# Performance work log

Hardware: AMD Instinct MI355X
Metric: run time of the kernel (lower is better)

## Reference

```python
import jax, jax.numpy as jnp
import numpy as np

D_MODEL, D_STATE, EXPAND = 1024, 256, 2
BATCH, SEQ = 8, 2048


def setup_inputs() -> dict:
    key = jax.random.key(0)
    ks = jax.random.split(key, 7)
    s = 0.02
    return {
        "x": jax.random.normal(ks[0], (BATCH, SEQ, D_MODEL), jnp.float32),
        "W_in": jax.random.normal(ks[1], (D_MODEL, D_MODEL * EXPAND), jnp.float32) * s,
        "b_in": jax.random.normal(ks[2], (D_MODEL * EXPAND,), jnp.float32) * s,
        "W_state": jax.random.normal(ks[3], (D_MODEL * EXPAND, D_STATE), jnp.float32) * s,
        "b_state": jax.random.normal(ks[4], (D_STATE,), jnp.float32) * s,
        "W_out": jax.random.normal(ks[5], (D_STATE, D_MODEL), jnp.float32) * s,
        "b_out": jax.random.normal(ks[6], (D_MODEL,), jnp.float32) * s,
        "init_state": jnp.zeros((1, D_STATE), jnp.float32),
    }


def reference(x, W_in, b_in, W_state, b_state, W_out, b_out, init_state):
    # x: [B, T, D]
    x_proj = jax.nn.silu(jnp.einsum("btd,de->bte", x, W_in) + b_in)  # [B,T,2D]
    # state_proj depends only on x_proj, so batch the GEMM over all timesteps
    updates = jnp.einsum("bte,es->bts", x_proj, W_state) + b_state    # [B,T,S]
    updates_t = jnp.swapaxes(updates, 0, 1)                            # [T,B,S]
    state0 = jnp.broadcast_to(init_state, (x.shape[0], init_state.shape[1]))

    def step(state, u):
        new = jax.nn.silu(state + u)
        return new, new

    _, states = jax.lax.scan(step, state0, updates_t)  # [T,B,S]
    out = jnp.einsum("tbs,sd->tbd", states, W_out) + b_out  # [T,B,D]
    return jnp.swapaxes(out, 0, 1)  # [B,T,D]
```

## Files before the change

### kernel.cpp

```cpp
#include <hip/hip_runtime.h>
#include <cstdint>
#include <cstddef>

#define BATCH 8
#define SEQ   2048
#define DM    1024
#define DE    2048
#define DSZ   256
#define MROWS (BATCH*SEQ)
#define MCHUNK 8192

typedef _Float16 f16;
typedef _Float16 f16x4 __attribute__((ext_vector_type(4)));
typedef _Float16 f16x8 __attribute__((ext_vector_type(8)));
typedef float  f32x4  __attribute__((ext_vector_type(4)));

__device__ __forceinline__ void glds16(const void* gp, void* lp) {
  __builtin_amdgcn_global_load_lds(
      (const __attribute__((address_space(1))) void*)gp,
      (__attribute__((address_space(3))) void*)lp, 16, 0, 0);
}

__device__ __forceinline__ float silu_f(float x) {
  return x * __builtin_amdgcn_rcpf(1.0f + __expf(-x));
}

__device__ __forceinline__ int swz(int k8, int r) { return k8 ^ ((r >> 1) & 3); }

__global__ void split_x_k(const float* __restrict__ in, f16* __restrict__ oh,
                          f16* __restrict__ ol, int n) {
  int i = (blockIdx.x * blockDim.x + threadIdx.x) * 4;
  const int stride = gridDim.x * blockDim.x * 4;
  for (; i < n; i += stride) {
    float4 v = *(const float4*)(in + i);
    f16x4 h, l;
    h[0] = (f16)v.x; l[0] = (f16)(v.x - (float)h[0]);
    h[1] = (f16)v.y; l[1] = (f16)(v.y - (float)h[1]);
    h[2] = (f16)v.z; l[2] = (f16)(v.z - (float)h[2]);
    h[3] = (f16)v.w; l[3] = (f16)(v.w - (float)h[3]);
    *(f16x4*)(oh + i) = h;
    *(f16x4*)(ol + i) = l;
  }
}

__global__ void transpose_split_k(const float* __restrict__ in, f16* __restrict__ oh,
                                  f16* __restrict__ ol, int R, int C) {
  __shared__ float tile[32][33];
  const int c0 = blockIdx.x * 32, r0 = blockIdx.y * 32;
  const int tx = threadIdx.x, ty = threadIdx.y;
  #pragma unroll
  for (int i = 0; i < 4; ++i)
    tile[ty + i*8][tx] = in[(size_t)(r0 + ty + i*8) * C + c0 + tx];
  __syncthreads();
  #pragma unroll
  for (int i = 0; i < 4; ++i) {
    float v = tile[tx][ty + i*8];
    f16 h = (f16)v;
    size_t idx = (size_t)(c0 + ty + i*8) * R + r0 + tx;
    oh[idx] = h;
    ol[idx] = (f16)(v - (float)h);
  }
}

__global__ void transpose_cast_f16_k(const float* __restrict__ in, f16* __restrict__ out, int R, int C) {
  __shared__ float tile[32][33];
  const int c0 = blockIdx.x * 32, r0 = blockIdx.y * 32;
  const int tx = threadIdx.x, ty = threadIdx.y;
  #pragma unroll
  for (int i = 0; i < 4; ++i)
    tile[ty + i*8][tx] = in[(size_t)(r0 + ty + i*8) * C + c0 + tx];
  __syncthreads();
  #pragma unroll
  for (int i = 0; i < 4; ++i)
    out[(size_t)(c0 + ty + i*8) * R + r0 + tx] = (f16)tile[tx][ty + i*8];
}

__global__ __launch_bounds__(512) void gemm1_k(const f16* __restrict__ Ah, const f16* __restrict__ Al,
                                               const f16* __restrict__ Bh, const f16* __restrict__ Bl,
                                               const float* __restrict__ bias,
                                               f16* __restrict__ Ch, f16* __restrict__ Cl) {
  const int K = 1024, N = 2048;
  __shared__ f16 sAh[2][4096], sAl[2][4096], sBh[2][4096], sBl[2][4096];

  const int tid = threadIdx.x;
  const int w = tid >> 6, l = tid & 63;
  const int bid = blockIdx.x;
  const int xcd = bid & 7, loc = bid >> 3;
  const int mt = xcd * 8 + (loc & 7);
  const int nt = loc >> 3;
  const int bm = mt * 128, bn = nt * 128;
  const int wm = (w >> 2) * 64, wn = (w & 3) * 32;
  const int lr = l & 15, lq = l >> 4;

  const int r = tid >> 2, k8 = swz(tid & 3, r);
  const f16* pAh = Ah + (size_t)(bm + r) * K + k8 * 8;
  const f16* pAl = Al + (size_t)(bm + r) * K + k8 * 8;
  const f16* pBh = Bh + (size_t)(bn + r) * K + k8 * 8;
  const f16* pBl = Bl + (size_t)(bn + r) * K + k8 * 8;
  const int dst = tid * 8;

  int offA[4], offB[2];
  #pragma unroll
  for (int i = 0; i < 4; ++i) {
    const int row = wm + i*16 + lr;
    offA[i] = row * 32 + swz(lq, row) * 8;
  }
  #pragma unroll
  for (int j = 0; j < 2; ++j) {
    const int row = wn + j*16 + lr;
    offB[j] = row * 32 + swz(lq, row) * 8;
  }

  f32x4 acc[4][2] = {};

  glds16(pAh, &sAh[0][dst]); glds16(pAl, &sAl[0][dst]);
  glds16(pBh, &sBh[0][dst]); glds16(pBl, &sBl[0][dst]);
  pAh += 32; pAl += 32; pBh += 32; pBl += 32;
  __syncthreads();

  for (int kt = 0; kt < 32; ++kt) {
    const int cur = kt & 1;
    if (kt < 31) {
      const int nxt = cur ^ 1;
      glds16(pAh, &sAh[nxt][dst]); glds16(pAl, &sAl[nxt][dst]);
      glds16(pBh, &sBh[nxt][dst]); glds16(pBl, &sBl[nxt][dst]);
      pAh += 32; pAl += 32; pBh += 32; pBl += 32;
    }
    f16x8 ah[4], al[4], bh[2], bl[2];
    #pragma unroll
    for (int i = 0; i < 4; ++i) {
      ah[i] = *(const f16x8*)(&sAh[cur][0] + offA[i]);
      al[i] = *(const f16x8*)(&sAl[cur][0] + offA[i]);
    }
    #pragma unroll
    for (int j = 0; j < 2; ++j) {
      bh[j] = *(const f16x8*)(&sBh[cur][0] + offB[j]);
      bl[j] = *(const f16x8*)(&sBl[cur][0] + offB[j]);
    }
    __builtin_amdgcn_s_setprio(1);
    #pragma unroll
    for (int i = 0; i < 4; ++i)
      #pragma unroll
      for (int j = 0; j < 2; ++j) {
        acc[i][j] = __builtin_amdgcn_mfma_f32_16x16x32_f16(ah[i], bh[j], acc[i][j], 0, 0, 0);
        acc[i][j] = __builtin_amdgcn_mfma_f32_16x16x32_f16(ah[i], bl[j], acc[i][j], 0, 0, 0);
        acc[i][j] = __builtin_amdgcn_mfma_f32_16x16x32_f16(al[i], bh[j], acc[i][j], 0, 0, 0);
      }
    __builtin_amdgcn_s_setprio(0);
    __syncthreads();
  }

  #pragma unroll
  for (int j = 0; j < 2; ++j) {
    const int col = bn + wn + j*16 + lr;
    const float bv = bias[col];
    #pragma unroll
    for (int i = 0; i < 4; ++i)
      #pragma unroll
      for (int r4 = 0; r4 < 4; ++r4) {
        const int row = bm + wm + i*16 + lq*4 + r4;
        const float s = silu_f(acc[i][j][r4] + bv);
        const f16 h = (f16)s;
        const size_t idx = (size_t)row * N + col;
        Ch[idx] = h;
        Cl[idx] = (f16)(s - (float)h);
      }
  }
}

__global__ __launch_bounds__(256) void gemm2s_k(const f16* __restrict__ Ah, const f16* __restrict__ Al,
                                                const f16* __restrict__ Bh, const f16* __restrict__ Bl,
                                                const float* __restrict__ bias,
                                                float* __restrict__ C) {
  const int K = 2048, N = 256;
  __shared__ f16 sAh[2][1024], sAl[2][1024], sBh[2][2048], sBl[2][2048];

  const int tid = threadIdx.x;
  const int w = tid >> 6, l = tid & 63;
  const int bid = blockIdx.x;
  const int bn = (bid >> 8) * 64;
  const int bm = (bid & 255) * 32;
  const int wm = (w & 1) * 16, wn = (w >> 1) * 32;
  const int lr = l & 15, lq = l >> 4;

  const int rB = tid >> 2, k8B = swz(tid & 3, rB);
  const f16* pBh = Bh + (size_t)(bn + rB) * K + k8B * 8;
  const f16* pBl = Bl + (size_t)(bn + rB) * K + k8B * 8;
  const int ca = tid & 127;
  const int rA = ca >> 2, k8A = swz(ca & 3, rA);
  const f16* pA = (tid < 128 ? Ah : Al) + (size_t)(bm + rA) * K + k8A * 8;
  const int dstB = tid * 8, dstA = ca * 8;

  int offA, offB[2];
  {
    const int row = wm + lr;
    offA = row * 32 + swz(lq, row) * 8;
  }
  #pragma unroll
  for (int j = 0; j < 2; ++j) {
    const int row = wn + j*16 + lr;
    offB[j] = row * 32 + swz(lq, row) * 8;
  }

  f32x4 acc[2] = {};

  glds16(pBh, &sBh[0][dstB]); glds16(pBl, &sBl[0][dstB]);
  glds16(pA, (tid < 128 ? &sAh[0][dstA] : &sAl[0][dstA]));
  pBh += 32; pBl += 32; pA += 32;
  __syncthreads();

  for (int kt = 0; kt < 64; ++kt) {
    const int cur = kt & 1;
    if (kt < 63) {
      const int nxt = cur ^ 1;
      glds16(pBh, &sBh[nxt][dstB]); glds16(pBl, &sBl[nxt][dstB]);
      glds16(pA, (tid < 128 ? &sAh[nxt][dstA] : &sAl[nxt][dstA]));
      pBh += 32; pBl += 32; pA += 32;
    }
    f16x8 ah, al, bh[2], bl[2];
    ah = *(const f16x8*)(&sAh[cur][0] + offA);
    al = *(const f16x8*)(&sAl[cur][0] + offA);
    #pragma unroll
    for (int j = 0; j < 2; ++j) {
      bh[j] = *(const f16x8*)(&sBh[cur][0] + offB[j]);
      bl[j] = *(const f16x8*)(&sBl[cur][0] + offB[j]);
    }
    __builtin_amdgcn_s_setprio(1);
    #pragma unroll
    for (int j = 0; j < 2; ++j) {
      acc[j] = __builtin_amdgcn_mfma_f32_16x16x32_f16(ah, bh[j], acc[j], 0, 0, 0);
      acc[j] = __builtin_amdgcn_mfma_f32_16x16x32_f16(ah, bl[j], acc[j], 0, 0, 0);
      acc[j] = __builtin_amdgcn_mfma_f32_16x16x32_f16(al, bh[j], acc[j], 0, 0, 0);
    }
    __builtin_amdgcn_s_setprio(0);
    __syncthreads();
  }

  #pragma unroll
  for (int j = 0; j < 2; ++j) {
    const int col = bn + wn + j*16 + lr;
    const float bv = bias[col];
    #pragma unroll
    for (int r4 = 0; r4 < 4; ++r4) {
      const int row = bm + wm + lq*4 + r4;
      C[(size_t)row * N + col] = acc[j][r4] + bv;
    }
  }
}

__global__ __launch_bounds__(256) void gemm3_k(const f16* __restrict__ A,
                                               const f16* __restrict__ Bt,
                                               const float* __restrict__ bias,
                                               float* __restrict__ C) {
  const int K = 256, N = 1024;
  __shared__ f16 sA[2][4096], sB[2][4096];

  const int tid = threadIdx.x;
  const int w = tid >> 6, l = tid & 63;
  const int bid = blockIdx.x;
  const int bm = (bid & 127) * 128, bn = (bid >> 7) * 128;
  const int wm = (w >> 1) * 64, wn = (w & 1) * 64;
  const int lr = l & 15, lq = l >> 4;

  const f16 *pA[2], *pB[2]; int dstc[2];
  #pragma unroll
  for (int p = 0; p < 2; ++p) {
    const int c = p * 256 + tid;
    const int r = c >> 2, k8 = swz(c & 3, r);
    pA[p] = A  + (size_t)(bm + r) * K + k8 * 8;
    pB[p] = Bt + (size_t)(bn + r) * K + k8 * 8;
    dstc[p] = c * 8;
  }

  int offA[4], offB[4];
  #pragma unroll
  for (int i = 0; i < 4; ++i) {
    const int rowA = wm + i*16 + lr;
    const int rowB = wn + i*16 + lr;
    offA[i] = rowA * 32 + swz(lq, rowA) * 8;
    offB[i] = rowB * 32 + swz(lq, rowB) * 8;
  }

  f32x4 acc[4][4] = {};

  glds16(pA[0], &sA[0][dstc[0]]); glds16(pA[1], &sA[0][dstc[1]]);
  glds16(pB[0], &sB[0][dstc[0]]); glds16(pB[1], &sB[0][dstc[1]]);
  pA[0] += 32; pA[1] += 32; pB[0] += 32; pB[1] += 32;
  __syncthreads();

  for (int kt = 0; kt < 8; ++kt) {
    const int cur = kt & 1;
    if (kt < 7) {
      const int nxt = cur ^ 1;
      glds16(pA[0], &sA[nxt][dstc[0]]); glds16(pA[1], &sA[nxt][dstc[1]]);
      glds16(pB[0], &sB[nxt][dstc[0]]); glds16(pB[1], &sB[nxt][dstc[1]]);
      pA[0] += 32; pA[1] += 32; pB[0] += 32; pB[1] += 32;
    }
    f16x8 af[4], bfr[4];
    #pragma unroll
    for (int i = 0; i < 4; ++i) af[i]  = *(const f16x8*)(&sA[cur][0] + offA[i]);
    #pragma unroll
    for (int j = 0; j < 4; ++j) bfr[j] = *(const f16x8*)(&sB[cur][0] + offB[j]);
    __builtin_amdgcn_s_setprio(1);
    #pragma unroll
    for (int i = 0; i < 4; ++i)
      #pragma unroll
      for (int j = 0; j < 4; ++j)
        acc[i][j] = __builtin_amdgcn_mfma_f32_16x16x32_f16(af[i], bfr[j], acc[i][j], 0, 0, 0);
    __builtin_amdgcn_s_setprio(0);
    __syncthreads();
  }

  #pragma unroll
  for (int j = 0; j < 4; ++j) {
    const int col = bn + wn + j*16 + lr;
    const float bv = bias[col];
    #pragma unroll
    for (int i = 0; i < 4; ++i)
      #pragma unroll
      for (int r4 = 0; r4 < 4; ++r4) {
        const int row = bm + wm + i*16 + lq*4 + r4;
        C[(size_t)row * N + col] = acc[i][j][r4] + bv;
      }
  }
}

#define L2E 1.4426950408889634f
__global__ __launch_bounds__(64) void scan_k(const float* __restrict__ upd,
                                             const float* __restrict__ init,
                                             f16* __restrict__ states) {
  const int b = blockIdx.x >> 2, sq = blockIdx.x & 3;
  const int s = sq * 64 + threadIdx.x;
  const float* u = upd + (size_t)b * SEQ * DSZ + s;
  f16* st = states + (size_t)b * SEQ * DSZ + s;
  float state = init[s];

  float r0[16], r1[16], r2[16], ulog[16];
  #pragma unroll
  for (int i = 0; i < 16; ++i) r0[i] = u[(size_t)i * DSZ];
  #pragma unroll
  for (int i = 0; i < 16; ++i) r1[i] = u[(size_t)(16 + i) * DSZ];
  #pragma unroll
  for (int i = 0; i < 16; ++i) ulog[i] = r0[i] * (-L2E);

  for (int t0 = 0; t0 < SEQ; t0 += 16) {
    if (t0 + 32 < SEQ) {
      #pragma unroll
      for (int i = 0; i < 16; ++i) r2[i] = u[(size_t)(t0 + 32 + i) * DSZ];
    }
    f16 res[16];
    #pragma unroll
    for (int i = 0; i < 16; ++i) {
      const float e = __builtin_amdgcn_exp2f(__builtin_fmaf(state, -L2E, ulog[i]));
      const float x = state + r0[i];
      state = x * __builtin_amdgcn_rcpf(1.0f + e);
      res[i] = (f16)state;
    }
    #pragma unroll
    for (int i = 0; i < 16; ++i) st[(size_t)(t0 + i) * DSZ] = res[i];
    #pragma unroll
    for (int i = 0; i < 16; ++i) { r0[i] = r1[i]; ulog[i] = r1[i] * (-L2E); r1[i] = r2[i]; }
  }
}

extern "C" void kernel_launch(void* const* d_in, const int* in_sizes, int n_in,
                              void* d_out, int out_size, void* d_ws, size_t ws_size,
                              hipStream_t stream) {
  const float* x       = (const float*)d_in[0];
  const float* W_in    = (const float*)d_in[1];
  const float* b_in    = (const float*)d_in[2];
  const float* W_state = (const float*)d_in[3];
  const float* b_state = (const float*)d_in[4];
  const float* W_out   = (const float*)d_in[5];
  const float* b_out   = (const float*)d_in[6];
  const float* init_st = (const float*)d_in[7];
  float* out = (float*)d_out;

  char* ws = (char*)d_ws;
  f16*   xh        = (f16*)(ws + 0);
  f16*   xl        = (f16*)(ws + 33554432);
  f16*   xproj_h   = (f16*)(ws + 67108864);
  f16*   xproj_l   = (f16*)(ws + 100663296);
  float* upd       = (float*)(ws + 134217728);
  f16*   states    = (f16*)(ws + 150994944);
  f16*   w_in_h    = (f16*)(ws + 159383552);
  f16*   w_in_l    = (f16*)(ws + 163577856);
  f16*   w_state_h = (f16*)(ws + 167772160);
  f16*   w_state_l = (f16*)(ws + 168820736);
  f16*   w_out_t   = (f16*)(ws + 169869312);

  split_x_k<<<4096, 256, 0, stream>>>(x, xh, xl, MROWS * DM);
  dim3 tb(32, 8);
  transpose_split_k<<<dim3(DE/32,  DM/32), tb, 0, stream>>>(W_in,    w_in_h,    w_in_l,    DM,  DE);
  transpose_split_k<<<dim3(DSZ/32, DE/32), tb, 0, stream>>>(W_state, w_state_h, w_state_l, DE,  DSZ);
  transpose_cast_f16_k<<<dim3(DM/32, DSZ/32), tb, 0, stream>>>(W_out, w_out_t, DSZ, DM);

  for (int c = 0; c < 2; ++c) {
    const size_t ro = (size_t)c * MCHUNK;
    gemm1_k<<<1024, 512, 0, stream>>>(
        xh + ro * DM, xl + ro * DM, w_in_h, w_in_l, b_in, xproj_h, xproj_l);
    gemm2s_k<<<1024, 256, 0, stream>>>(
        xproj_h, xproj_l, w_state_h, w_state_l, b_state, upd + ro * DSZ);
  }

  scan_k<<<BATCH*4, 64, 0, stream>>>(upd, init_st, states);

  gemm3_k<<<1024, 256, 0, stream>>>(states, w_out_t, b_out, out);
}
```

Baseline: 576.1 us.

## Enlarge gemm2 tile to 64x64 with 8 waves and split-K loads; remap gemm3 grid

The state-projection GEMM moves from 32x64 tiles with 4 waves to 64x64 tiles with 8 waves. The two halves of the block load alternate 32-wide K slices, so each barrier covers a 64-wide K step and there are half as many sync iterations. Weight tiles are reused across more rows, which cuts redundant global loads of B, at the cost of more LDS per block. The output GEMM also gets a 2D grid whose x dimension walks N, which changes block rasterization so consecutive blocks share A rows.

```diff
diff --git a/kernel.cpp b/kernel.cpp
--- a/kernel.cpp
+++ b/kernel.cpp
@@ -168,28 +168,29 @@
   }
 }
 
-__global__ __launch_bounds__(256) void gemm2s_k(const f16* __restrict__ Ah, const f16* __restrict__ Al,
+__global__ __launch_bounds__(512) void gemm2s_k(const f16* __restrict__ Ah, const f16* __restrict__ Al,
                                                 const f16* __restrict__ Bh, const f16* __restrict__ Bl,
                                                 const float* __restrict__ bias,
                                                 float* __restrict__ C) {
   const int K = 2048, N = 256;
-  __shared__ f16 sAh[2][1024], sAl[2][1024], sBh[2][2048], sBl[2][2048];
+  __shared__ f16 sAh[2][2][2048], sAl[2][2][2048], sBh[2][2][2048], sBl[2][2][2048];
 
   const int tid = threadIdx.x;
   const int w = tid >> 6, l = tid & 63;
   const int bid = blockIdx.x;
-  const int bn = (bid >> 8) * 64;
-  const int bm = (bid & 255) * 32;
-  const int wm = (w & 1) * 16, wn = (w >> 1) * 32;
+  const int bm = (bid & 127) * 64;
+  const int bn = (bid >> 7) * 64;
+  const int wm = (w >> 1) * 16, wn = (w & 1) * 32;
   const int lr = l & 15, lq = l >> 4;
 
-  const int rB = tid >> 2, k8B = swz(tid & 3, rB);
-  const f16* pBh = Bh + (size_t)(bn + rB) * K + k8B * 8;
-  const f16* pBl = Bl + (size_t)(bn + rB) * K + k8B * 8;
-  const int ca = tid & 127;
-  const int rA = ca >> 2, k8A = swz(ca & 3, rA);
-  const f16* pA = (tid < 128 ? Ah : Al) + (size_t)(bm + rA) * K + k8A * 8;
-  const int dstB = tid * 8, dstA = ca * 8;
+  const int c = tid & 255, s = tid >> 8;
+  const int r = c >> 2, k8 = swz(c & 3, r);
+  const size_t koff = (size_t)s * 32 + k8 * 8;
+  const f16* pAh = Ah + (size_t)(bm + r) * K + koff;
+  const f16* pAl = Al + (size_t)(bm + r) * K + koff;
+  const f16* pBh = Bh + (size_t)(bn + r) * K + koff;
+  const f16* pBl = Bl + (size_t)(bn + r) * K + koff;
+  const int dst = c * 8;
 
   int offA, offB[2];
   {
@@ -204,35 +205,38 @@
 
   f32x4 acc[2] = {};
 
-  glds16(pBh, &sBh[0][dstB]); glds16(pBl, &sBl[0][dstB]);
-  glds16(pA, (tid < 128 ? &sAh[0][dstA] : &sAl[0][dstA]));
-  pBh += 32; pBl += 32; pA += 32;
+  glds16(pAh, &sAh[0][s][dst]); glds16(pAl, &sAl[0][s][dst]);
+  glds16(pBh, &sBh[0][s][dst]); glds16(pBl, &sBl[0][s][dst]);
+  pAh += 64; pAl += 64; pBh += 64; pBl += 64;
   __syncthreads();
 
-  for (int kt = 0; kt < 64; ++kt) {
+  for (int kt = 0; kt < 32; ++kt) {
     const int cur = kt & 1;
-    if (kt < 63) {
+    if (kt < 31) {
       const int nxt = cur ^ 1;
-      glds16(pBh, &sBh[nxt][dstB]); glds16(pBl, &sBl[nxt][dstB]);
-      glds16(pA, (tid < 128 ? &sAh[nxt][dstA] : &sAl[nxt][dstA]));
-      pBh += 32; pBl += 32; pA += 32;
-    }
-    f16x8 ah, al, bh[2], bl[2];
-    ah = *(const f16x8*)(&sAh[cur][0] + offA);
-    al = *(const f16x8*)(&sAl[cur][0] + offA);
-    #pragma unroll
-    for (int j = 0; j < 2; ++j) {
-      bh[j] = *(const f16x8*)(&sBh[cur][0] + offB[j]);
-      bl[j] = *(const f16x8*)(&sBl[cur][0] + offB[j]);
-    }
-    __builtin_amdgcn_s_setprio(1);
-    #pragma unroll
-    for (int j = 0; j < 2; ++j) {
-      acc[j] = __builtin_amdgcn_mfma_f32_16x16x32_f16(ah, bh[j], acc[j], 0, 0, 0);
-      acc[j] = __builtin_amdgcn_mfma_f32_16x16x32_f16(ah, bl[j], acc[j], 0, 0, 0);
-      acc[j] = __builtin_amdgcn_mfma_f32_16x16x32_f16(al, bh[j], acc[j], 0, 0, 0);
-    }
-    __builtin_amdgcn_s_setprio(0);
+      glds16(pAh, &sAh[nxt][s][dst]); glds16(pAl, &sAl[nxt][s][dst]);
+      glds16(pBh, &sBh[nxt][s][dst]); glds16(pBl, &sBl[nxt][s][dst]);
+      pAh += 64; pAl += 64; pBh += 64; pBl += 64;
+    }
+    #pragma unroll
+    for (int ss = 0; ss < 2; ++ss) {
+      f16x8 ah, al, bh[2], bl[2];
+      ah = *(const f16x8*)(&sAh[cur][ss][0] + offA);
+      al = *(const f16x8*)(&sAl[cur][ss][0] + offA);
+      #pragma unroll
+      for (int j = 0; j < 2; ++j) {
+        bh[j] = *(const f16x8*)(&sBh[cur][ss][0] + offB[j]);
+        bl[j] = *(const f16x8*)(&sBl[cur][ss][0] + offB[j]);
+      }
+      __builtin_amdgcn_s_setprio(1);
+      #pragma unroll
+      for (int j = 0; j < 2; ++j) {
+        acc[j] = __builtin_amdgcn_mfma_f32_16x16x32_f16(ah, bh[j], acc[j], 0, 0, 0);
+        acc[j] = __builtin_amdgcn_mfma_f32_16x16x32_f16(ah, bl[j], acc[j], 0, 0, 0);
+        acc[j] = __builtin_amdgcn_mfma_f32_16x16x32_f16(al, bh[j], acc[j], 0, 0, 0);
+      }
+      __builtin_amdgcn_s_setprio(0);
+    }
     __syncthreads();
   }
 
@@ -257,8 +261,7 @@
 
   const int tid = threadIdx.x;
   const int w = tid >> 6, l = tid & 63;
-  const int bid = blockIdx.x;
-  const int bm = (bid & 127) * 128, bn = (bid >> 7) * 128;
+  const int bm = blockIdx.y * 128, bn = blockIdx.x * 128;
   const int wm = (w >> 1) * 64, wn = (w & 1) * 64;
   const int lr = l & 15, lq = l >> 4;
 
@@ -399,11 +402,11 @@
     const size_t ro = (size_t)c * MCHUNK;
     gemm1_k<<<1024, 512, 0, stream>>>(
         xh + ro * DM, xl + ro * DM, w_in_h, w_in_l, b_in, xproj_h, xproj_l);
-    gemm2s_k<<<1024, 256, 0, stream>>>(
+    gemm2s_k<<<512, 512, 0, stream>>>(
         xproj_h, xproj_l, w_state_h, w_state_l, b_state, upd + ro * DSZ);
   }
 
   scan_k<<<BATCH*4, 64, 0, stream>>>(upd, init_st, states);
 
-  gemm3_k<<<1024, 256, 0, stream>>>(states, w_out_t, b_out, out);
-}
+  gemm3_k<<<dim3(DM/128, MROWS/128), 256, 0, stream>>>(states, w_out_t, b_out, out);
+}
```

Result: faster. 533.5 us, median of 2 (-7.4%).
